# Kernel tuning notes

Measured on AMD Instinct MI355X. Metric: run time of the kernel, lower is better.

The kernel has to match this reference:

```python
import jax, jax.numpy as jnp
import numpy as np

N_NODES = 50000
DEG = 16
N_EDGES = N_NODES * DEG
NDIM = 128
EDIM = 128
HEADS = 8
DIM = max(NDIM, EDIM)
DK = DIM // HEADS
FFN_HID = 4 * NDIM
EPS = 1e-5


def _ln(h, g, b):
    m = h.mean(-1, keepdims=True)
    v = ((h - m) ** 2).mean(-1, keepdims=True)
    return (h - m) / jnp.sqrt(v + EPS) * g + b


def setup_inputs() -> dict:
    key = jax.random.key(0)
    ks = jax.random.split(key, 12)
    x = jax.random.normal(ks[0], (N_NODES, NDIM), jnp.float32)
    lgx = jax.random.normal(ks[1], (N_EDGES, EDIM), jnp.float32)
    # every node gets DEG incoming edges (sorted dst), random sources
    edge_dst = jnp.repeat(jnp.arange(N_NODES, dtype=jnp.int32), DEG)
    edge_src = jax.random.randint(ks[2], (N_EDGES,), 0, N_NODES, jnp.int32)
    s = 1.0 / np.sqrt(NDIM)
    Wq = jax.random.uniform(ks[3], (DIM, NDIM), jnp.float32, -s, s)
    bq = jnp.zeros((DIM,), jnp.float32)
    Wk = jax.random.uniform(ks[4], (DIM, NDIM), jnp.float32, -s, s)
    Wv = jax.random.uniform(ks[5], (DIM, NDIM), jnp.float32, -s, s)
    so = 1.0 / np.sqrt(DIM)
    Wo = jax.random.uniform(ks[6], (NDIM, DIM), jnp.float32, -so, so)
    bo = jnp.zeros((NDIM,), jnp.float32)
    ln1_g = jnp.ones((NDIM,), jnp.float32); ln1_b = jnp.zeros((NDIM,), jnp.float32)
    W1 = jax.random.uniform(ks[7], (FFN_HID, NDIM), jnp.float32, -s, s)
    b1 = jnp.zeros((FFN_HID,), jnp.float32)
    sh = 1.0 / np.sqrt(FFN_HID)
    W2 = jax.random.uniform(ks[8], (NDIM, FFN_HID), jnp.float32, -sh, sh)
    b2 = jnp.zeros((NDIM,), jnp.float32)
    ln2_g = jnp.ones((NDIM,), jnp.float32); ln2_b = jnp.zeros((NDIM,), jnp.float32)
    return dict(x=x, lgx=lgx, edge_src=edge_src, edge_dst=edge_dst,
                Wq=Wq, bq=bq, Wk=Wk, Wv=Wv, Wo=Wo, bo=bo,
                ln1_g=ln1_g, ln1_b=ln1_b, W1=W1, b1=b1, W2=W2, b2=b2,
                ln2_g=ln2_g, ln2_b=ln2_b)


def reference(x, lgx, edge_src, edge_dst, Wq, bq, Wk, Wv, Wo, bo,
              ln1_g, ln1_b, W1, b1, W2, b2, ln2_g, ln2_b):
    N = x.shape[0]
    # projections (dropout is identity in eval mode)
    q = (x @ Wq.T + bq).reshape(N, HEADS, DK)
    k = (x @ Wk.T).reshape(N, HEADS, DK)
    v = (x @ Wv.T).reshape(N, HEADS, DK)
    e = lgx.reshape(-1, HEADS, DK)  # edim == dim branch
    # edge scores: ((k_src + e) * q_dst).sum(-1), scaled-exp with clamp
    score = jnp.einsum('ehd,ehd->eh', k[edge_src] + e, q[edge_dst])
    score = jnp.exp(jnp.clip(score / np.sqrt(DK), -10.0, 10.0))  # [E,H]
    # weighted message aggregation and softmax normalization
    msg = (v[edge_src] + e) * score[:, :, None]  # [E,H,DK]
    wv = jax.ops.segment_sum(msg, edge_dst, num_segments=N)   # [N,H,DK]
    z = jax.ops.segment_sum(score, edge_dst, num_segments=N)  # [N,H]
    o = wv / z[:, :, None]
    h = _ln(x + o.reshape(N, HEADS * DK) @ Wo.T + bo, ln1_g, ln1_b)
    # residual FFN
    out = _ln(h + jax.nn.relu(h @ W1.T + b1) @ W2.T + b2, ln2_g, ln2_b)
    return out
```

## Files before the change

kernel.cpp:

```cpp
#include <hip/hip_runtime.h>


typedef unsigned short bf16;
typedef unsigned int uint;
typedef __attribute__((ext_vector_type(8))) short short8;
typedef __attribute__((ext_vector_type(4))) float f32x4;

#define NN 50000
#define DEG 16
#define NTILE 16
#define MT 32

__device__ __forceinline__ float blo(uint u) { return __uint_as_float(u << 16); }
__device__ __forceinline__ float bhi(uint u) { return __uint_as_float(u & 0xffff0000u); }

__device__ __forceinline__ uint f2bfbits(float f) {
  uint u = __float_as_uint(f);
  return (u + 0x7fffu + ((u >> 16) & 1u)) >> 16;
}
__device__ __forceinline__ uint pack2(float a, float b) {
  return f2bfbits(a) | (f2bfbits(b) << 16);
}
__device__ __forceinline__ void unpack8(uint4 r, float* f) {
  f[0] = blo(r.x); f[1] = bhi(r.x);
  f[2] = blo(r.y); f[3] = bhi(r.y);
  f[4] = blo(r.z); f[5] = bhi(r.z);
  f[6] = blo(r.w); f[7] = bhi(r.w);
}
__device__ __forceinline__ float fma4(float4 w, float4 v, float acc) {
  acc = fmaf(w.x, v.x, acc); acc = fmaf(w.y, v.y, acc);
  acc = fmaf(w.z, v.z, acc); acc = fmaf(w.w, v.w, acc);
  return acc;
}

__global__ __launch_bounds__(256) void k_prep(
    const float* __restrict__ W1, const float* __restrict__ W2,
    bf16* __restrict__ W1b, bf16* __restrict__ W2b) {
  int i = (blockIdx.x * 256 + threadIdx.x) * 4;
  float4 a = *(const float4*)(W1 + i);
  float4 b = *(const float4*)(W2 + i);
  *(uint2*)(W1b + i) = make_uint2(pack2(a.x, a.y), pack2(a.z, a.w));
  *(uint2*)(W2b + i) = make_uint2(pack2(b.x, b.y), pack2(b.z, b.w));
}

__global__ __launch_bounds__(64) void k_qkv(
    const float* __restrict__ x, const float* __restrict__ Wq,
    const float* __restrict__ bq, const float* __restrict__ Wk,
    const float* __restrict__ Wv, bf16* __restrict__ qkv) {
  const int n0 = blockIdx.x * NTILE;
  const int t = threadIdx.x;
  const int d0 = 2 * t;
  __shared__ float4 xs4[NTILE * 32];
  {
    const float4* xg = (const float4*)(x + (size_t)n0 * 128);
    for (int i = t; i < NTILE * 32; i += 64) xs4[i] = xg[i];
  }
  __syncthreads();
  float aq0[NTILE], aq1[NTILE], ak0[NTILE], ak1[NTILE], av0[NTILE], av1[NTILE];
#pragma unroll
  for (int i = 0; i < NTILE; ++i) { aq0[i]=0.f; aq1[i]=0.f; ak0[i]=0.f; ak1[i]=0.f; av0[i]=0.f; av1[i]=0.f; }
  const float4* pq0 = (const float4*)(Wq + (size_t)d0 * 128);
  const float4* pq1 = (const float4*)(Wq + (size_t)(d0 + 1) * 128);
  const float4* pk0 = (const float4*)(Wk + (size_t)d0 * 128);
  const float4* pk1 = (const float4*)(Wk + (size_t)(d0 + 1) * 128);
  const float4* pv0 = (const float4*)(Wv + (size_t)d0 * 128);
  const float4* pv1 = (const float4*)(Wv + (size_t)(d0 + 1) * 128);
  for (int c = 0; c < 32; ++c) {
    float4 wq0 = pq0[c], wq1 = pq1[c];
    float4 wk0 = pk0[c], wk1 = pk1[c];
    float4 wv0 = pv0[c], wv1 = pv1[c];
#pragma unroll
    for (int i = 0; i < NTILE; ++i) {
      float4 xr = xs4[i * 32 + c];
      aq0[i] = fma4(wq0, xr, aq0[i]); aq1[i] = fma4(wq1, xr, aq1[i]);
      ak0[i] = fma4(wk0, xr, ak0[i]); ak1[i] = fma4(wk1, xr, ak1[i]);
      av0[i] = fma4(wv0, xr, av0[i]); av1[i] = fma4(wv1, xr, av1[i]);
    }
  }
  float2 bqv = *(const float2*)(bq + d0);
  for (int i = 0; i < NTILE; ++i) {
    size_t base = (size_t)(n0 + i) * 384;
    *(uint*)(qkv + base + d0)       = pack2(aq0[i] + bqv.x, aq1[i] + bqv.y);
    *(uint*)(qkv + base + 128 + d0) = pack2(ak0[i], ak1[i]);
    *(uint*)(qkv + base + 256 + d0) = pack2(av0[i], av1[i]);
  }
}

__global__ __launch_bounds__(64) void k_attn(
    const float* __restrict__ x, const float* __restrict__ lgx,
    const int* __restrict__ esrc, const bf16* __restrict__ qkv,
    const float* __restrict__ Wo, const float* __restrict__ bo,
    const float* __restrict__ g1, const float* __restrict__ b1l,
    bf16* __restrict__ hbuf) {
  const int n0 = blockIdx.x * NTILE;
  const int t = threadIdx.x;
  const int d0 = 2 * t;
  __shared__ float4 ot4[NTILE * 32];
  __shared__ float vt[NTILE][132];
  __shared__ float lnm[NTILE], lnr[NTILE];

  for (int i = 0; i < NTILE; ++i) {
    const int n = n0 + i;
    uint qraw = *(const uint*)(qkv + (size_t)n * 384 + d0);
    float q0 = blo(qraw), q1 = bhi(qraw);
    float wv0 = 0.f, wv1 = 0.f, z = 0.f;
#pragma unroll 4
    for (int j = 0; j < DEG; ++j) {
      size_t e = (size_t)n * DEG + j;
      int s = esrc[e];
      uint kraw = *(const uint*)(qkv + (size_t)s * 384 + 128 + d0);
      uint vraw = *(const uint*)(qkv + (size_t)s * 384 + 256 + d0);
      float2 ev = *(const float2*)(lgx + e * 128 + d0);
      float tt = (blo(kraw) + ev.x) * q0 + (bhi(kraw) + ev.y) * q1;
      tt += __shfl_xor(tt, 1); tt += __shfl_xor(tt, 2); tt += __shfl_xor(tt, 4);
      float sc = expf(fminf(fmaxf(tt * 0.25f, -10.f), 10.f));
      wv0 = fmaf(blo(vraw) + ev.x, sc, wv0);
      wv1 = fmaf(bhi(vraw) + ev.y, sc, wv1);
      z += sc;
    }
    float iz = 1.f / z;
    ((float2*)ot4)[i * 64 + t] = make_float2(wv0 * iz, wv1 * iz);
  }
  __syncthreads();
  float a0[NTILE], a1[NTILE];
#pragma unroll
  for (int i = 0; i < NTILE; ++i) { a0[i] = 0.f; a1[i] = 0.f; }
  const float4* p0 = (const float4*)(Wo + (size_t)d0 * 128);
  const float4* p1 = (const float4*)(Wo + (size_t)(d0 + 1) * 128);
  for (int c = 0; c < 32; ++c) {
    float4 w0 = p0[c], w1 = p1[c];
#pragma unroll
    for (int i = 0; i < NTILE; ++i) {
      float4 orv = ot4[i * 32 + c];
      a0[i] = fma4(w0, orv, a0[i]); a1[i] = fma4(w1, orv, a1[i]);
    }
  }
  float2 bov = *(const float2*)(bo + d0);
  for (int i = 0; i < NTILE; ++i) {
    float2 xr = *(const float2*)(x + (size_t)(n0 + i) * 128 + d0);
    vt[i][d0]     = a0[i] + bov.x + xr.x;
    vt[i][d0 + 1] = a1[i] + bov.y + xr.y;
  }
  __syncthreads();
  {
    int r = t >> 2, qq = t & 3;
    float s = 0.f, s2 = 0.f;
#pragma unroll
    for (int i = 0; i < 32; ++i) { float v = vt[r][qq + 4 * i]; s += v; s2 += v * v; }
    s += __shfl_xor(s, 1); s2 += __shfl_xor(s2, 1);
    s += __shfl_xor(s, 2); s2 += __shfl_xor(s2, 2);
    if (qq == 0) {
      float m = s * 0.0078125f;
      lnm[r] = m;
      lnr[r] = rsqrtf(s2 * 0.0078125f - m * m + 1e-5f);
    }
  }
  __syncthreads();
  float2 gv = *(const float2*)(g1 + d0);
  float2 cv = *(const float2*)(b1l + d0);
  for (int i = 0; i < NTILE; ++i) {
    float o0 = (vt[i][d0] - lnm[i]) * lnr[i] * gv.x + cv.x;
    float o1 = (vt[i][d0 + 1] - lnm[i]) * lnr[i] * gv.y + cv.y;
    *(uint*)(hbuf + (size_t)(n0 + i) * 128 + d0) = pack2(o0, o1);
  }
}

__global__ __launch_bounds__(256) void k_ffn(
    const bf16* __restrict__ hbuf, const bf16* __restrict__ W1b,
    const float* __restrict__ b1, const bf16* __restrict__ W2b,
    const float* __restrict__ b2, const float* __restrict__ g2,
    const float* __restrict__ b2l, float* __restrict__ out) {
  const int n0 = blockIdx.x * MT;
  const int t = threadIdx.x;
  const int w = t >> 6, l = t & 63;
  const int lr = l & 15, lk = l >> 4;

  __shared__ __align__(16) char hs[MT * 256];
  __shared__ __align__(16) char hidb[MT * 1024];
  float (*vt)[132] = (float (*)[132])hidb;
  __shared__ float lnm[MT], lnr[MT];

  {
    int r = t >> 3, seg = t & 7;
    int node = n0 + r; if (node >= NN) node = NN - 1;
    const uint4* src = (const uint4*)(hbuf + (size_t)node * 128 + seg * 16);
    uint4 h0 = src[0], h1 = src[1];
    const int swz = (r & 7) << 4;
    *(uint4*)(hs + r * 256 + ((seg * 32) ^ swz))      = h0;
    *(uint4*)(hs + r * 256 + ((seg * 32 + 16) ^ swz)) = h1;
  }
  __syncthreads();

  f32x4 acc1[2][8];
#pragma unroll
  for (int mi = 0; mi < 2; ++mi)
#pragma unroll
    for (int ni = 0; ni < 8; ++ni) acc1[mi][ni] = (f32x4){0.f, 0.f, 0.f, 0.f};
#pragma unroll
  for (int kk = 0; kk < 4; ++kk) {
    const int kb = kk * 64 + lk * 16;
    const int r0 = lr, r1 = 16 + lr;
    short8 a0 = *(const short8*)(hs + r0 * 256 + (kb ^ ((r0 & 7) << 4)));
    short8 a1 = *(const short8*)(hs + r1 * 256 + (kb ^ ((r1 & 7) << 4)));
#pragma unroll
    for (int ni = 0; ni < 8; ++ni) {
      int col = w * 128 + ni * 16 + lr;
      short8 b = *(const short8*)(W1b + (size_t)col * 128 + kk * 32 + lk * 8);
      acc1[0][ni] = __builtin_amdgcn_mfma_f32_16x16x32_bf16(a0, b, acc1[0][ni], 0, 0, 0);
      acc1[1][ni] = __builtin_amdgcn_mfma_f32_16x16x32_bf16(a1, b, acc1[1][ni], 0, 0, 0);
    }
  }
#pragma unroll
  for (int ni = 0; ni < 8; ++ni) {
    int col = w * 128 + ni * 16 + lr;
    float bias = b1[col];
#pragma unroll
    for (int mi = 0; mi < 2; ++mi)
#pragma unroll
      for (int r = 0; r < 4; ++r) {
        int row = mi * 16 + lk * 4 + r;
        float v = fmaxf(acc1[mi][ni][r] + bias, 0.f);
        *(unsigned short*)(hidb + row * 1024 + ((col * 2) ^ ((row & 7) << 4))) =
            (unsigned short)f2bfbits(v);
      }
  }
  __syncthreads();

  f32x4 acc2[2][2];
#pragma unroll
  for (int mi = 0; mi < 2; ++mi)
#pragma unroll
    for (int ni = 0; ni < 2; ++ni) acc2[mi][ni] = (f32x4){0.f, 0.f, 0.f, 0.f};
#pragma unroll 4
  for (int kk = 0; kk < 16; ++kk) {
    const int kb = kk * 64 + lk * 16;
    const int r0 = lr, r1 = 16 + lr;
    short8 a0 = *(const short8*)(hidb + r0 * 1024 + (kb ^ ((r0 & 7) << 4)));
    short8 a1 = *(const short8*)(hidb + r1 * 1024 + (kb ^ ((r1 & 7) << 4)));
#pragma unroll
    for (int ni = 0; ni < 2; ++ni) {
      int col = w * 32 + ni * 16 + lr;
      short8 b = *(const short8*)(W2b + (size_t)col * 512 + kk * 32 + lk * 8);
      acc2[0][ni] = __builtin_amdgcn_mfma_f32_16x16x32_bf16(a0, b, acc2[0][ni], 0, 0, 0);
      acc2[1][ni] = __builtin_amdgcn_mfma_f32_16x16x32_bf16(a1, b, acc2[1][ni], 0, 0, 0);
    }
  }
  __syncthreads();

#pragma unroll
  for (int ni = 0; ni < 2; ++ni) {
    int col = w * 32 + ni * 16 + lr;
    float bias = b2[col];
#pragma unroll
    for (int mi = 0; mi < 2; ++mi)
#pragma unroll
      for (int r = 0; r < 4; ++r) {
        int row = mi * 16 + lk * 4 + r;
        uint hb = *(const unsigned short*)(hs + row * 256 + ((col * 2) ^ ((row & 7) << 4)));
        vt[row][col] = acc2[mi][ni][r] + bias + __uint_as_float(hb << 16);
      }
  }
  __syncthreads();

  {
    int r = t >> 3, qq = t & 7;
    float s = 0.f, s2 = 0.f;
#pragma unroll
    for (int i = 0; i < 16; ++i) { float v = vt[r][qq + 8 * i]; s += v; s2 += v * v; }
    s += __shfl_xor(s, 1); s2 += __shfl_xor(s2, 1);
    s += __shfl_xor(s, 2); s2 += __shfl_xor(s2, 2);
    s += __shfl_xor(s, 4); s2 += __shfl_xor(s2, 4);
    if (qq == 0) {
      float m = s * 0.0078125f;
      lnm[r] = m;
      lnr[r] = rsqrtf(s2 * 0.0078125f - m * m + 1e-5f);
    }
  }
  __syncthreads();

  {
    int r = t >> 3, seg = t & 7;
    int node = n0 + r;
    if (node < NN) {
      float m = lnm[r], ir = lnr[r];
#pragma unroll
      for (int j0 = 0; j0 < 16; j0 += 4) {
        int c = seg * 16 + j0;
        float4 gv = *(const float4*)(g2 + c);
        float4 cv = *(const float4*)(b2l + c);
        float4 o;
        o.x = (vt[r][c + 0] - m) * ir * gv.x + cv.x;
        o.y = (vt[r][c + 1] - m) * ir * gv.y + cv.y;
        o.z = (vt[r][c + 2] - m) * ir * gv.z + cv.z;
        o.w = (vt[r][c + 3] - m) * ir * gv.w + cv.w;
        *(float4*)(out + (size_t)node * 128 + c) = o;
      }
    }
  }
}

extern "C" void kernel_launch(void* const* d_in, const int* in_sizes, int n_in,
                              void* d_out, int out_size, void* d_ws, size_t ws_size,
                              hipStream_t stream) {
  const float* x   = (const float*)d_in[0];
  const float* lgx = (const float*)d_in[1];
  const int* esrc  = (const int*)d_in[2];
  const float* Wq  = (const float*)d_in[4];
  const float* bq  = (const float*)d_in[5];
  const float* Wk  = (const float*)d_in[6];
  const float* Wv  = (const float*)d_in[7];
  const float* Wo  = (const float*)d_in[8];
  const float* bo  = (const float*)d_in[9];
  const float* g1  = (const float*)d_in[10];
  const float* b1l = (const float*)d_in[11];
  const float* W1  = (const float*)d_in[12];
  const float* b1  = (const float*)d_in[13];
  const float* W2  = (const float*)d_in[14];
  const float* b2  = (const float*)d_in[15];
  const float* g2  = (const float*)d_in[16];
  const float* b2l = (const float*)d_in[17];

  bf16* qkv  = (bf16*)d_ws;
  bf16* hbuf = qkv + (size_t)NN * 384;
  bf16* W1b  = hbuf + (size_t)NN * 128;
  bf16* W2b  = W1b + 512 * 128;
  float* outp = (float*)d_out;

  const int nblk = NN / NTILE;
  const int fblk = (NN + MT - 1) / MT;
  k_prep<<<dim3(64), dim3(256), 0, stream>>>(W1, W2, W1b, W2b);
  k_qkv<<<dim3(nblk), dim3(64), 0, stream>>>(x, Wq, bq, Wk, Wv, qkv);
  k_attn<<<dim3(nblk), dim3(64), 0, stream>>>(x, lgx, esrc, qkv, Wo, bo, g1, b1l, hbuf);
  k_ffn<<<dim3(fblk), dim3(256), 0, stream>>>(hbuf, W1b, b1, W2b, b2, g2, b2l, outp);
}
```

Measured before the change: 875.4 us.

## Use bf16 MFMA for QKV and output projections with pre-converted weights

Converts Wq/Wk/Wv/Wo to bf16 in the prep kernel. The scalar fp32 FMA loops in the QKV kernel and the attention kernel's Wo projection are replaced with 16x16x32 bf16 MFMA tiles, using an XOR-swizzled LDS layout for the activations. The QKV kernel now processes 32 nodes per 256-thread block, and the edge-source indices are loaded as vectors up front. The aim is to offload the dense GEMM work from the vector ALUs, at the cost of bf16 rounding of x and the attention output before projection.

Measured after the change: 734.1 us. -16.1%, faster.

```diff
diff --git a/kernel.cpp b/kernel.cpp
--- a/kernel.cpp
+++ b/kernel.cpp
@@ -21,93 +21,114 @@
 __device__ __forceinline__ uint pack2(float a, float b) {
   return f2bfbits(a) | (f2bfbits(b) << 16);
 }
-__device__ __forceinline__ void unpack8(uint4 r, float* f) {
-  f[0] = blo(r.x); f[1] = bhi(r.x);
-  f[2] = blo(r.y); f[3] = bhi(r.y);
-  f[4] = blo(r.z); f[5] = bhi(r.z);
-  f[6] = blo(r.w); f[7] = bhi(r.w);
-}
-__device__ __forceinline__ float fma4(float4 w, float4 v, float acc) {
-  acc = fmaf(w.x, v.x, acc); acc = fmaf(w.y, v.y, acc);
-  acc = fmaf(w.z, v.z, acc); acc = fmaf(w.w, v.w, acc);
-  return acc;
-}
 
 __global__ __launch_bounds__(256) void k_prep(
     const float* __restrict__ W1, const float* __restrict__ W2,
-    bf16* __restrict__ W1b, bf16* __restrict__ W2b) {
-  int i = (blockIdx.x * 256 + threadIdx.x) * 4;
-  float4 a = *(const float4*)(W1 + i);
-  float4 b = *(const float4*)(W2 + i);
-  *(uint2*)(W1b + i) = make_uint2(pack2(a.x, a.y), pack2(a.z, a.w));
-  *(uint2*)(W2b + i) = make_uint2(pack2(b.x, b.y), pack2(b.z, b.w));
-}
-
-__global__ __launch_bounds__(64) void k_qkv(
-    const float* __restrict__ x, const float* __restrict__ Wq,
-    const float* __restrict__ bq, const float* __restrict__ Wk,
-    const float* __restrict__ Wv, bf16* __restrict__ qkv) {
-  const int n0 = blockIdx.x * NTILE;
+    const float* __restrict__ Wq, const float* __restrict__ Wk,
+    const float* __restrict__ Wv, const float* __restrict__ Wo,
+    bf16* __restrict__ W1b, bf16* __restrict__ W2b,
+    bf16* __restrict__ Wqkvb, bf16* __restrict__ Wob) {
+  int b = blockIdx.x;
+  const float* src; bf16* dst; int base;
+  if (b < 64)       { src = W1; dst = W1b;           base = b; }
+  else if (b < 128) { src = W2; dst = W2b;           base = b - 64; }
+  else if (b < 144) { src = Wq; dst = Wqkvb;         base = b - 128; }
+  else if (b < 160) { src = Wk; dst = Wqkvb + 16384; base = b - 144; }
+  else if (b < 176) { src = Wv; dst = Wqkvb + 32768; base = b - 160; }
+  else              { src = Wo; dst = Wob;           base = b - 176; }
+  int i = (base * 256 + (int)threadIdx.x) * 4;
+  float4 a = *(const float4*)(src + i);
+  *(uint2*)(dst + i) = make_uint2(pack2(a.x, a.y), pack2(a.z, a.w));
+}
+
+__global__ __launch_bounds__(256) void k_qkv(
+    const float* __restrict__ x, const bf16* __restrict__ Wqkvb,
+    const float* __restrict__ bq, bf16* __restrict__ qkv) {
+  const int n0 = blockIdx.x * MT;
   const int t = threadIdx.x;
-  const int d0 = 2 * t;
-  __shared__ float4 xs4[NTILE * 32];
-  {
-    const float4* xg = (const float4*)(x + (size_t)n0 * 128);
-    for (int i = t; i < NTILE * 32; i += 64) xs4[i] = xg[i];
-  }
-  __syncthreads();
-  float aq0[NTILE], aq1[NTILE], ak0[NTILE], ak1[NTILE], av0[NTILE], av1[NTILE];
-#pragma unroll
-  for (int i = 0; i < NTILE; ++i) { aq0[i]=0.f; aq1[i]=0.f; ak0[i]=0.f; ak1[i]=0.f; av0[i]=0.f; av1[i]=0.f; }
-  const float4* pq0 = (const float4*)(Wq + (size_t)d0 * 128);
-  const float4* pq1 = (const float4*)(Wq + (size_t)(d0 + 1) * 128);
-  const float4* pk0 = (const float4*)(Wk + (size_t)d0 * 128);
-  const float4* pk1 = (const float4*)(Wk + (size_t)(d0 + 1) * 128);
-  const float4* pv0 = (const float4*)(Wv + (size_t)d0 * 128);
-  const float4* pv1 = (const float4*)(Wv + (size_t)(d0 + 1) * 128);
-  for (int c = 0; c < 32; ++c) {
-    float4 wq0 = pq0[c], wq1 = pq1[c];
-    float4 wk0 = pk0[c], wk1 = pk1[c];
-    float4 wv0 = pv0[c], wv1 = pv1[c];
-#pragma unroll
-    for (int i = 0; i < NTILE; ++i) {
-      float4 xr = xs4[i * 32 + c];
-      aq0[i] = fma4(wq0, xr, aq0[i]); aq1[i] = fma4(wq1, xr, aq1[i]);
-      ak0[i] = fma4(wk0, xr, ak0[i]); ak1[i] = fma4(wk1, xr, ak1[i]);
-      av0[i] = fma4(wv0, xr, av0[i]); av1[i] = fma4(wv1, xr, av1[i]);
-    }
-  }
-  float2 bqv = *(const float2*)(bq + d0);
-  for (int i = 0; i < NTILE; ++i) {
-    size_t base = (size_t)(n0 + i) * 384;
-    *(uint*)(qkv + base + d0)       = pack2(aq0[i] + bqv.x, aq1[i] + bqv.y);
-    *(uint*)(qkv + base + 128 + d0) = pack2(ak0[i], ak1[i]);
-    *(uint*)(qkv + base + 256 + d0) = pack2(av0[i], av1[i]);
+  const int w = t >> 6, l = t & 63;
+  const int lr = l & 15, lk = l >> 4;
+  __shared__ __align__(16) char xs[MT * 256];
+
+  {
+    int r = t >> 3, seg = t & 7;
+    int node = n0 + r; if (node >= NN) node = NN - 1;
+    const float4* src = (const float4*)(x + (size_t)node * 128 + seg * 16);
+    float4 a = src[0], b = src[1], c = src[2], d = src[3];
+    uint4 h0 = make_uint4(pack2(a.x, a.y), pack2(a.z, a.w), pack2(b.x, b.y), pack2(b.z, b.w));
+    uint4 h1 = make_uint4(pack2(c.x, c.y), pack2(c.z, c.w), pack2(d.x, d.y), pack2(d.z, d.w));
+    const int swz = (r & 7) << 4;
+    *(uint4*)(xs + r * 256 + ((seg * 32) ^ swz))      = h0;
+    *(uint4*)(xs + r * 256 + ((seg * 32 + 16) ^ swz)) = h1;
+  }
+  __syncthreads();
+
+  f32x4 acc[2][6];
+#pragma unroll
+  for (int mi = 0; mi < 2; ++mi)
+#pragma unroll
+    for (int j = 0; j < 6; ++j) acc[mi][j] = (f32x4){0.f, 0.f, 0.f, 0.f};
+#pragma unroll
+  for (int kk = 0; kk < 4; ++kk) {
+    const int kb = kk * 64 + lk * 16;
+    const int r0 = lr, r1 = 16 + lr;
+    short8 a0 = *(const short8*)(xs + r0 * 256 + (kb ^ ((r0 & 7) << 4)));
+    short8 a1 = *(const short8*)(xs + r1 * 256 + (kb ^ ((r1 & 7) << 4)));
+#pragma unroll
+    for (int j = 0; j < 6; ++j) {
+      int f = w + 4 * j;
+      short8 b = *(const short8*)(Wqkvb + (size_t)(f * 16 + lr) * 128 + kk * 32 + lk * 8);
+      acc[0][j] = __builtin_amdgcn_mfma_f32_16x16x32_bf16(a0, b, acc[0][j], 0, 0, 0);
+      acc[1][j] = __builtin_amdgcn_mfma_f32_16x16x32_bf16(a1, b, acc[1][j], 0, 0, 0);
+    }
+  }
+#pragma unroll
+  for (int j = 0; j < 6; ++j) {
+    int f = w + 4 * j;
+    int col = f * 16 + lr;
+    float bias = 0.f;
+    if (col < 128) bias = bq[col];
+#pragma unroll
+    for (int mi = 0; mi < 2; ++mi)
+#pragma unroll
+      for (int r = 0; r < 4; ++r) {
+        int row = mi * 16 + lk * 4 + r;
+        int node = n0 + row;
+        if (node < NN)
+          qkv[(size_t)node * 384 + col] = (bf16)f2bfbits(acc[mi][j][r] + bias);
+      }
   }
 }
 
 __global__ __launch_bounds__(64) void k_attn(
     const float* __restrict__ x, const float* __restrict__ lgx,
     const int* __restrict__ esrc, const bf16* __restrict__ qkv,
-    const float* __restrict__ Wo, const float* __restrict__ bo,
+    const bf16* __restrict__ Wob, const float* __restrict__ bo,
     const float* __restrict__ g1, const float* __restrict__ b1l,
     bf16* __restrict__ hbuf) {
   const int n0 = blockIdx.x * NTILE;
   const int t = threadIdx.x;
   const int d0 = 2 * t;
-  __shared__ float4 ot4[NTILE * 32];
+  const int lr = t & 15, lk = t >> 4;
+  __shared__ __align__(16) char obuf[NTILE * 256];
   __shared__ float vt[NTILE][132];
   __shared__ float lnm[NTILE], lnr[NTILE];
 
   for (int i = 0; i < NTILE; ++i) {
     const int n = n0 + i;
+    int4 e0 = *(const int4*)(esrc + (size_t)n * DEG);
+    int4 e1 = *(const int4*)(esrc + (size_t)n * DEG + 4);
+    int4 e2 = *(const int4*)(esrc + (size_t)n * DEG + 8);
+    int4 e3 = *(const int4*)(esrc + (size_t)n * DEG + 12);
+    int es[16] = {e0.x, e0.y, e0.z, e0.w, e1.x, e1.y, e1.z, e1.w,
+                  e2.x, e2.y, e2.z, e2.w, e3.x, e3.y, e3.z, e3.w};
     uint qraw = *(const uint*)(qkv + (size_t)n * 384 + d0);
     float q0 = blo(qraw), q1 = bhi(qraw);
     float wv0 = 0.f, wv1 = 0.f, z = 0.f;
-#pragma unroll 4
+#pragma unroll 8
     for (int j = 0; j < DEG; ++j) {
       size_t e = (size_t)n * DEG + j;
-      int s = esrc[e];
+      int s = es[j];
       uint kraw = *(const uint*)(qkv + (size_t)s * 384 + 128 + d0);
       uint vraw = *(const uint*)(qkv + (size_t)s * 384 + 256 + d0);
       float2 ev = *(const float2*)(lgx + e * 128 + d0);
@@ -119,27 +140,32 @@
       z += sc;
     }
     float iz = 1.f / z;
-    ((float2*)ot4)[i * 64 + t] = make_float2(wv0 * iz, wv1 * iz);
-  }
-  __syncthreads();
-  float a0[NTILE], a1[NTILE];
-#pragma unroll
-  for (int i = 0; i < NTILE; ++i) { a0[i] = 0.f; a1[i] = 0.f; }
-  const float4* p0 = (const float4*)(Wo + (size_t)d0 * 128);
-  const float4* p1 = (const float4*)(Wo + (size_t)(d0 + 1) * 128);
-  for (int c = 0; c < 32; ++c) {
-    float4 w0 = p0[c], w1 = p1[c];
-#pragma unroll
-    for (int i = 0; i < NTILE; ++i) {
-      float4 orv = ot4[i * 32 + c];
-      a0[i] = fma4(w0, orv, a0[i]); a1[i] = fma4(w1, orv, a1[i]);
-    }
-  }
-  float2 bov = *(const float2*)(bo + d0);
-  for (int i = 0; i < NTILE; ++i) {
-    float2 xr = *(const float2*)(x + (size_t)(n0 + i) * 128 + d0);
-    vt[i][d0]     = a0[i] + bov.x + xr.x;
-    vt[i][d0 + 1] = a1[i] + bov.y + xr.y;
+    *(uint*)(obuf + i * 256 + ((4 * t) ^ ((i & 7) << 4))) = pack2(wv0 * iz, wv1 * iz);
+  }
+  __syncthreads();
+
+  f32x4 acc[8];
+#pragma unroll
+  for (int ni = 0; ni < 8; ++ni) acc[ni] = (f32x4){0.f, 0.f, 0.f, 0.f};
+#pragma unroll
+  for (int kk = 0; kk < 4; ++kk) {
+    const int kb = kk * 64 + lk * 16;
+    short8 a = *(const short8*)(obuf + lr * 256 + (kb ^ ((lr & 7) << 4)));
+#pragma unroll
+    for (int ni = 0; ni < 8; ++ni) {
+      short8 b = *(const short8*)(Wob + (size_t)(ni * 16 + lr) * 128 + kk * 32 + lk * 8);
+      acc[ni] = __builtin_amdgcn_mfma_f32_16x16x32_bf16(a, b, acc[ni], 0, 0, 0);
+    }
+  }
+#pragma unroll
+  for (int ni = 0; ni < 8; ++ni) {
+    int col = ni * 16 + lr;
+    float bias = bo[col];
+#pragma unroll
+    for (int r = 0; r < 4; ++r) {
+      int row = lk * 4 + r;
+      vt[row][col] = acc[ni][r] + bias + x[(size_t)(n0 + row) * 128 + col];
+    }
   }
   __syncthreads();
   {
@@ -320,16 +346,18 @@
   const float* g2  = (const float*)d_in[16];
   const float* b2l = (const float*)d_in[17];
 
-  bf16* qkv  = (bf16*)d_ws;
-  bf16* hbuf = qkv + (size_t)NN * 384;
-  bf16* W1b  = hbuf + (size_t)NN * 128;
-  bf16* W2b  = W1b + 512 * 128;
+  bf16* qkv   = (bf16*)d_ws;
+  bf16* hbuf  = qkv + (size_t)NN * 384;
+  bf16* W1b   = hbuf + (size_t)NN * 128;
+  bf16* W2b   = W1b + 512 * 128;
+  bf16* Wqkvb = W2b + 128 * 512;
+  bf16* Wob   = Wqkvb + 3 * 128 * 128;
   float* outp = (float*)d_out;
 
   const int nblk = NN / NTILE;
-  const int fblk = (NN + MT - 1) / MT;
-  k_prep<<<dim3(64), dim3(256), 0, stream>>>(W1, W2, W1b, W2b);
-  k_qkv<<<dim3(nblk), dim3(64), 0, stream>>>(x, Wq, bq, Wk, Wv, qkv);
-  k_attn<<<dim3(nblk), dim3(64), 0, stream>>>(x, lgx, esrc, qkv, Wo, bo, g1, b1l, hbuf);
-  k_ffn<<<dim3(fblk), dim3(256), 0, stream>>>(hbuf, W1b, b1, W2b, b2, g2, b2l, outp);
-}
+  const int mblk = (NN + MT - 1) / MT;
+  k_prep<<<dim3(192), dim3(256), 0, stream>>>(W1, W2, Wq, Wk, Wv, Wo, W1b, W2b, Wqkvb, Wob);
+  k_qkv<<<dim3(mblk), dim3(256), 0, stream>>>(x, Wqkvb, bq, qkv);
+  k_attn<<<dim3(nblk), dim3(64), 0, stream>>>(x, lgx, esrc, qkv, Wob, bo, g1, b1l, hbuf);
+  k_ffn<<<dim3(mblk), dim3(256), 0, stream>>>(hbuf, W1b, b1, W2b, b2, g2, b2l, outp);
+}
```
